# Kernel tuning notes

Hardware: AMD Instinct MI355X
Metric: run time of the kernel (lower is better)

## Reference

```python
import jax, jax.numpy as jnp
import numpy as np

# Forest of complete L-ary trees, BFS level-contiguous node numbering.
B_TREES, ARITY, DEPTH = 8, 4, 8
C, M, NGEN = 8, 100, 4
COUNTS = [B_TREES * ARITY**l for l in range(DEPTH + 1)]
OFFS = np.concatenate([[0], np.cumsum(COUNTS)]).astype(np.int64)
DIM = int(OFFS[-1])  # 699048
# tree id of each node: within-level index // (ARITY**level)
BATCH = np.concatenate([np.arange(COUNTS[l]) // (ARITY**l) for l in range(DEPTH + 1)])


def setup_inputs() -> dict:
    key = jax.random.key(0)
    k1, k2, k3, k4 = jax.random.split(key, 4)
    return {
        "x": jax.random.randint(k1, (DIM,), 0, M, dtype=jnp.int32),
        "A": jax.random.normal(k2, (C, C, ARITY, NGEN), dtype=jnp.float32) * 2.5,
        "B_emit": jax.random.normal(k3, (C, M, NGEN), dtype=jnp.float32) * 2.5,
        "Pi": jax.random.normal(k4, (C, NGEN), dtype=jnp.float32) * 2.5,
    }


def _htmm_loglik(x, A, B_emit, Pi):
    # softmax reparameterization (matches F.softmax axes in torch code)
    smA = jax.nn.softmax(A, axis=0)            # [C,C,L,G], over child state
    smA_t = jnp.transpose(smA, (2, 0, 1, 3))   # [L,C,C,G]
    smB = jax.nn.softmax(B_emit, axis=1)       # [C,M,G]
    smPi = jax.nn.softmax(Pi, axis=0)          # [C,G]

    # preliminary downward: prior state distribution per node, level by level.
    # Children of a parent are contiguous with sibling position j = idx % ARITY.
    prior_lvls = [jnp.broadcast_to(smPi, (COUNTS[0], C, NGEN))]
    for l in range(1, DEPTH + 1):
        n_pa = COUNTS[l - 1]
        # prior_child[c] = sum_d A[c, d, pos_j, g] * prior_pa[d]
        pl = jnp.einsum('jcdg,pdg->pjcg', smA_t, prior_lvls[-1])
        prior_lvls.append(pl.reshape(n_pa * ARITY, C, NGEN))
    prior = jnp.concatenate(prior_lvls, axis=0)  # [DIM,C,G]

    em = jnp.transpose(smB[:, x], (1, 0, 2))     # [DIM,C,G]
    beta0 = prior * em

    ll = jnp.zeros((DIM, NGEN), dtype=beta0.dtype)
    # leaves = deepest level
    beta_lvl = beta0[OFFS[DEPTH]:OFFS[DEPTH + 1]]
    nu = beta_lvl.sum(1)                          # [n_leaves,G]
    beta_lvl = beta_lvl / nu[:, None, :]
    ll = ll.at[OFFS[DEPTH]:OFFS[DEPTH + 1]].set(jnp.log(nu))

    # upward recursion, bottom-up
    for l in range(DEPTH, 0, -1):
        n_pa = COUNTS[l - 1]
        ratio = (beta_lvl / prior[OFFS[l]:OFFS[l + 1]]).reshape(n_pa, ARITY, C, NGEN)
        # beta_uv[d] = sum_c A[c, d, pos_j, g] * beta_ch[c] / prior_ch[c]
        beta_uv = jnp.einsum('jcdg,pjcg->pjdg', smA_t, ratio)  # [n_pa,L,C,G]
        beta_pa = beta0[OFFS[l - 1]:OFFS[l]] * jnp.prod(beta_uv, axis=1)
        nu = beta_pa.sum(1)
        beta_lvl = beta_pa / nu[:, None, :]
        ll = ll.at[OFFS[l - 1]:OFFS[l]].set(jnp.log(nu))

    # scatter per-node log-likelihood contributions into per-tree totals
    return jax.ops.segment_sum(ll, jnp.asarray(BATCH), num_segments=B_TREES)  # [B_TREES,G]


def reference(x, A, B_emit, Pi):
    return _htmm_loglik(x, A, B_emit, Pi)
```

## Files before the change

kernel.cpp:

```cpp
#include <hip/hip_runtime.h>

constexpr int OFFS1 = 8, OFFS2 = 40, OFFS3 = 168, OFFS4 = 680;
constexpr int OFFS5 = 2728, OFFS6 = 10920, OFFS7 = 43688, OFFS8 = 174760;


template <int CTRL>
static __device__ __forceinline__ float dppmov(float v) {
  return __int_as_float(__builtin_amdgcn_update_dpp(0, __float_as_int(v), CTRL, 0xF, 0xF, true));
}

static __device__ __forceinline__ float bfly8(float v) {
  v += dppmov<0xB1>(v);
  v += dppmov<0x4E>(v);
  v += dppmov<0x141>(v);
  return v;
}

static __device__ __forceinline__ void oct8(float v, float pv[8]) {
  float m = dppmov<0x141>(v);
  pv[0] = dppmov<0x00>(v); pv[1] = dppmov<0x55>(v);
  pv[2] = dppmov<0xAA>(v); pv[3] = dppmov<0xFF>(v);
  pv[4] = dppmov<0x00>(m); pv[5] = dppmov<0x55>(m);
  pv[6] = dppmov<0xAA>(m); pv[7] = dppmov<0xFF>(m);
}

static __device__ __forceinline__ float dot8(const float w[8], const float v[8]) {
  return w[0]*v[0] + w[1]*v[1] + w[2]*v[2] + w[3]*v[3] +
         w[4]*v[4] + w[5]*v[5] + w[6]*v[6] + w[7]*v[7];
}

static __device__ __forceinline__ void ld8p(const float* p, float wp[8], int h) {
  const float4* q = (const float4*)p;
  float4 a = q[h], b = q[1 - h];
  wp[0] = a.x; wp[1] = a.y; wp[2] = a.z; wp[3] = a.w;
  wp[4] = b.w; wp[5] = b.z; wp[6] = b.y; wp[7] = b.x;
}

static __device__ __forceinline__ float dot8p(const float wp[8], const float* p, int h) {
  const float4* q = (const float4*)p;
  float4 a = q[h], b = q[1 - h];
  return wp[0]*a.x + wp[1]*a.y + wp[2]*a.z + wp[3]*a.w +
         wp[4]*b.w + wp[5]*b.z + wp[6]*b.y + wp[7]*b.x;
}

static __device__ __forceinline__ float dot8pT(const float wp[8], const float* row, int h) {
  const float2* q = (const float2*)row;
  float2 a = q[2 * h], b = q[2 * h + 1], c = q[3 - 2 * h], d = q[2 - 2 * h];
  return wp[0]*a.x + wp[1]*a.y + wp[2]*b.x + wp[3]*b.y +
         wp[4]*c.y + wp[5]*c.x + wp[6]*d.y + wp[7]*d.x;
}

static __device__ __forceinline__ float rcpf(float x) { return __builtin_amdgcn_rcpf(x); }

static __device__ __forceinline__ float step_downT(const float* wtdT, float v, int j,
                                                   int sg, int h) {
  float pv[8];
  oct8(v, pv);
  return dot8pT(pv, &wtdT[(j * 32 + sg) * 10], h);
}

static __device__ __forceinline__ float step_down(const float* wtd_l, float v, int j,
                                                  int r, int h) {
  const float* wb = &wtd_l[j * 256 + r];
  float w[8];
#pragma unroll
  for (int k = 0; k < 4; k++) {
    w[k]     = wb[(4 * h + k) * 32];
    w[4 + k] = wb[(7 - 4 * h - k) * 32];
  }
  float pv[8];
  oct8(v, pv);
  return dot8(w, pv);
}

static __device__ __forceinline__ float upprod(const float wup_p[4][8], const float rat[4]) {
  float prod = 1.f;
#pragma unroll
  for (int j = 0; j < 4; j++) {
    float pr[8];
    oct8(rat[j], pr);
    prod *= dot8(wup_p[j], pr);
  }
  return prod;
}

static __device__ __forceinline__ float leaf7(float u7, float e0, float e1, float e2,
                                              float e3, float em, float* acc) {
  float n0 = bfly8(u7 * e0), n1 = bfly8(u7 * e1);
  float n2 = bfly8(u7 * e2), n3 = bfly8(u7 * e3);
  float p01 = n0 * n1, p23 = n2 * n3;
  float prod = (e0 * e1 * rcpf(p01)) * (e2 * e3 * rcpf(p23));
  *acc += __logf(p01) + __logf(p23);
  float nu7 = bfly8(u7 * em * prod);
  *acc += __logf(nu7);
  return em * prod * rcpf(nu7);
}

static __device__ __forceinline__ void build_tables(const float* __restrict__ A,
                                                    const float* __restrict__ Bm,
                                                    const float* __restrict__ Pi,
                                                    float* wtd_l, float* emt_l,
                                                    float* pit_l, float* llb, int t) {
  if (t < 128) {
    int d = t >> 4, j = (t >> 2) & 3, gg = t & 3;
    float v[8], sum = 0.f;
#pragma unroll
    for (int ss = 0; ss < 8; ss++) { v[ss] = __expf(A[((ss * 8 + d) * 4 + j) * 4 + gg]); sum += v[ss]; }
    float inv = rcpf(sum);
#pragma unroll
    for (int ss = 0; ss < 8; ss++) wtd_l[(j * 8 + d) * 32 + gg * 8 + ss] = v[ss] * inv;
  }
  if (t < 4) {
    float v[8], sum = 0.f;
#pragma unroll
    for (int c = 0; c < 8; c++) { v[c] = __expf(Pi[c * 4 + t]); sum += v[c]; }
    float inv = rcpf(sum);
#pragma unroll
    for (int c = 0; c < 8; c++) pit_l[t * 8 + c] = v[c] * inv;
    llb[t] = 0.f;
  }
  {
    int row = t >> 3, part = t & 7, c = row >> 2, gg = row & 3;
    int m0 = part < 4 ? part * 13 : 52 + (part - 4) * 12;
    int mn = part < 4 ? 13 : 12;
    float sum = 0.f;
    for (int m = m0; m < m0 + mn; m++) sum += __expf(Bm[(c * 100 + m) * 4 + gg]);
    sum = bfly8(sum);
    float inv = rcpf(sum);
    for (int m = m0; m < m0 + mn; m++)
      emt_l[m * 32 + gg * 8 + c] = __expf(Bm[(c * 100 + m) * 4 + gg]) * inv;
  }
}

__global__ __launch_bounds__(256, 2) void k_phase1(const int* __restrict__ x,
                                                   const float* __restrict__ A,
                                                   const float* __restrict__ Bm,
                                                   const float* __restrict__ Pi,
                                                   float* __restrict__ RAT4,
                                                   float* __restrict__ blocksum) {
  __shared__ __align__(16) float wtd_l[1024];
  __shared__ __align__(16) float wtdT[1280];
  __shared__ __align__(16) float emt_l[3200];
  __shared__ __align__(16) float pit_l[32];
  __shared__ __align__(16) float xb[320];
  __shared__ float llb[4];

  int t = threadIdx.x;
  int r = t & 31, g = r >> 3, s = r & 7, grp = t >> 5;
  int h = s >> 2, gb = g * 8;
  int sg = s * 4 + g;
  int b = blockIdx.x;

  build_tables(A, Bm, Pi, wtd_l, emt_l, pit_l, llb, t);
  __syncthreads();
  if (t < 128) {
    int j = t >> 5, ss = (t >> 2) & 7, gg = t & 3;
#pragma unroll
    for (int d = 0; d < 8; d++) wtdT[t * 10 + d] = wtd_l[(j * 8 + d) * 32 + gg * 8 + ss];
  }
  float wup_p[4][8];
#pragma unroll
  for (int j = 0; j < 4; j++) ld8p(&wtd_l[(j * 8 + s) * 32 + gb], wup_p[j], h);
  __syncthreads();

  float acc = 0.f;
  {
    int n5 = b * 8 + grp;
    const int4* x8v = (const int4*)(x + OFFS8 + n5 * 64);
    const int4* x7p = (const int4*)(x + OFFS7 + n5 * 16);
    int4 x6v = *(const int4*)(x + OFFS6 + n5 * 4);
    int x5s = x[OFFS5 + n5];
    const int* x6a = (const int*)&x6v;

    float v5 = pit_l[r], pri4 = 0.f;
#pragma unroll
    for (int k = 1; k <= 5; k++) {
      v5 = step_downT(wtdT, v5, (n5 >> (2 * (5 - k))) & 3, sg, h);
      if (k == 4) pri4 = v5;
    }
    float pv5[8];
    oct8(v5, pv5);

    float rat6[4];
#pragma unroll
    for (int q6 = 0; q6 < 4; q6++) {
      float u6 = dot8pT(pv5, &wtdT[(q6 * 32 + sg) * 10], h);
      float pv6[8];
      oct8(u6, pv6);
      int4 x7q = x7p[q6];
      const int* x7a = (const int*)&x7q;

      float rat7[4];
#pragma unroll
      for (int q7 = 0; q7 < 4; q7++) {
        int4 xl = x8v[q6 * 4 + q7];
        const int* xa = (const int*)&xl;
        float E[4];
#pragma unroll
        for (int j = 0; j < 4; j++) E[j] = dot8p(wup_p[j], &emt_l[xa[j] * 32 + gb], h);
        float u7 = dot8pT(pv6, &wtdT[(q7 * 32 + sg) * 10], h);
        rat7[q7] = leaf7(u7, E[0], E[1], E[2], E[3], emt_l[x7a[q7] * 32 + r], &acc);
      }
      float prod6 = upprod(wup_p, rat7);
      float em6 = emt_l[x6a[q6] * 32 + r];
      float nu6 = bfly8(u6 * em6 * prod6);
      acc += __logf(nu6);
      rat6[q6] = em6 * prod6 * rcpf(nu6);
    }
    float prod5 = upprod(wup_p, rat6);
    float em5 = emt_l[x5s * 32 + r];
    float nu5 = bfly8(v5 * em5 * prod5);
    acc += __logf(nu5);
    xb[grp * 32 + r] = em5 * prod5 * rcpf(nu5);
    if ((grp & 3) == 0) xb[256 + (grp >> 2) * 32 + r] = pri4;
  }
  __syncthreads();

  if (grp < 2) {
    int n4 = b * 2 + grp;
    float prod = 1.f;
#pragma unroll
    for (int j = 0; j < 4; j++) prod *= dot8p(wup_p[j], &xb[(grp * 4 + j) * 32 + gb], h);
    float em = emt_l[x[OFFS4 + n4] * 32 + r];
    float pr4 = xb[256 + grp * 32 + r];
    float nu = bfly8(pr4 * em * prod);
    acc += __logf(nu);
    RAT4[n4 * 32 + r] = em * prod * rcpf(nu);
  }

  if (s == 0) atomicAdd(&llb[g], acc);
  __syncthreads();
  if (t < 4) blocksum[b * 4 + t] = llb[t];
}

__global__ __launch_bounds__(256) void k_phase2(const int* __restrict__ x,
                                                const float* __restrict__ A,
                                                const float* __restrict__ Bm,
                                                const float* __restrict__ Pi,
                                                const float* __restrict__ RAT4,
                                                const float* __restrict__ blocksum,
                                                float* __restrict__ out) {
  __shared__ __align__(16) float wtd_l[1024];
  __shared__ __align__(16) float emt_l[3200];
  __shared__ __align__(16) float pit_l[32];
  __shared__ __align__(16) float stg[8192];
  __shared__ __align__(16) float xb[640];
  __shared__ float llb[4];

  int t = threadIdx.x;
  int r = t & 31, g = r >> 3, s = r & 7, grp = t >> 5;
  int h = s >> 2, gb = g * 8;
  int tree = blockIdx.x;

  build_tables(A, Bm, Pi, wtd_l, emt_l, pit_l, llb, t);
  {
    const float4* src = (const float4*)(RAT4 + tree * 8192);
    float4* dst = (float4*)stg;
#pragma unroll
    for (int i = 0; i < 8; i++) dst[i * 256 + t] = src[i * 256 + t];
  }
  __syncthreads();

  float wtd_p[4][8], wup_p[4][8];
#pragma unroll
  for (int j = 0; j < 4; j++) {
    const float* wb = &wtd_l[j * 256 + r];
#pragma unroll
    for (int k = 0; k < 4; k++) {
      wtd_p[j][k]     = wb[(4 * h + k) * 32];
      wtd_p[j][4 + k] = wb[(7 - 4 * h - k) * 32];
    }
    ld8p(&wtd_l[(j * 8 + s) * 32 + gb], wup_p[j], h);
  }

  float acc2 = 0.f;
  {
    int n2A = tree * 16 + grp, n2B = n2A + 8;
    int4 x3A = *(const int4*)(x + OFFS3 + n2A * 4);
    int4 x3B = *(const int4*)(x + OFFS3 + n2B * 4);
    int x2A = x[OFFS2 + n2A], x2B = x[OFFS2 + n2B];
    const int* xa = (const int*)&x3A;
    const int* xbv = (const int*)&x3B;
    float v2A = pit_l[r], v2B = v2A;
    v2A = step_down(wtd_l, v2A, (n2A >> 2) & 3, r, h);
    v2B = step_down(wtd_l, v2B, (n2B >> 2) & 3, r, h);
    v2A = step_down(wtd_l, v2A, n2A & 3, r, h);
    v2B = step_down(wtd_l, v2B, n2B & 3, r, h);
    float pv2A[8], pv2B[8];
    oct8(v2A, pv2A); oct8(v2B, pv2B);
    float rat3A[4], rat3B[4];
#pragma unroll
    for (int j3 = 0; j3 < 4; j3++) {
      int i3A = grp * 4 + j3, i3B = (8 + grp) * 4 + j3;
      float p3A = dot8(wtd_p[j3], pv2A);
      float p3B = dot8(wtd_p[j3], pv2B);
      float prodA = 1.f, prodB = 1.f;
#pragma unroll
      for (int j = 0; j < 4; j++) {
        prodA *= dot8p(wup_p[j], &stg[(i3A * 4 + j) * 32 + gb], h);
        prodB *= dot8p(wup_p[j], &stg[(i3B * 4 + j) * 32 + gb], h);
      }
      float emA = emt_l[xa[j3] * 32 + r], emB = emt_l[xbv[j3] * 32 + r];
      float nuA = bfly8(p3A * emA * prodA), nuB = bfly8(p3B * emB * prodB);
      acc2 += __logf(nuA) + __logf(nuB);
      rat3A[j3] = emA * prodA * rcpf(nuA);
      rat3B[j3] = emB * prodB * rcpf(nuB);
    }
    float prodA = upprod(wup_p, rat3A);
    float prodB = upprod(wup_p, rat3B);
    float emA = emt_l[x2A * 32 + r], emB = emt_l[x2B * 32 + r];
    float nuA = bfly8(v2A * emA * prodA), nuB = bfly8(v2B * emB * prodB);
    acc2 += __logf(nuA) + __logf(nuB);
    xb[grp * 32 + r] = emA * prodA * rcpf(nuA);
    xb[(8 + grp) * 32 + r] = emB * prodB * rcpf(nuB);
  }
  __syncthreads();
  if (grp < 4) {
    int n1g = tree * 4 + grp;
    float v1 = step_down(wtd_l, pit_l[r], grp, r, h);
    float prod = 1.f;
#pragma unroll
    for (int j = 0; j < 4; j++) prod *= dot8p(wup_p[j], &xb[(grp * 4 + j) * 32 + gb], h);
    float em = emt_l[x[OFFS1 + n1g] * 32 + r];
    float nu = bfly8(v1 * em * prod);
    acc2 += __logf(nu);
    xb[512 + grp * 32 + r] = em * prod * rcpf(nu);
  }
  __syncthreads();
  if (grp == 0) {
    float pr = pit_l[r];
    float prod = 1.f;
#pragma unroll
    for (int j = 0; j < 4; j++) prod *= dot8p(wup_p[j], &xb[512 + j * 32 + gb], h);
    float em = emt_l[x[tree] * 32 + r];
    float nu = bfly8(pr * em * prod);
    acc2 += __logf(nu);
  }
  __syncthreads();
  if (s == 0) atomicAdd(&llb[g], acc2);
  float v = blocksum[tree * 512 + t] + blocksum[tree * 512 + 256 + t];
  __syncthreads();
  stg[t] = v;
  __syncthreads();
#pragma unroll
  for (int off = 128; off >= 4; off >>= 1) {
    if (t < off) stg[t] += stg[t + off];
    __syncthreads();
  }
  if (t < 4) out[tree * 4 + t] = stg[t] + llb[t];
}

extern "C" void kernel_launch(void* const* d_in, const int* in_sizes, int n_in,
                              void* d_out, int out_size, void* d_ws, size_t ws_size,
                              hipStream_t stream) {
  const int* x = (const int*)d_in[0];
  const float* A = (const float*)d_in[1];
  const float* Bm = (const float*)d_in[2];
  const float* Pi = (const float*)d_in[3];
  float* ws = (float*)d_ws;
  float* blocksum = ws + 256;
  float* RAT4 = ws + 256 + 4096;
  float* out = (float*)d_out;

  k_phase1<<<1024, 256, 0, stream>>>(x, A, Bm, Pi, RAT4, blocksum);
  k_phase2<<<8, 256, 0, stream>>>(x, A, Bm, Pi, RAT4, blocksum, out);
}
```

Measured before the change: 100.1 us.

## Stage x indices in LDS, stream upward products, and stop unrolling phase1 loops

Phase1 now loads the block's x indices for levels 5-8 into shared memory with coalesced loads at the start, instead of issuing per-wave int4 global loads inside the loop. The upward product is accumulated on the fly with a new transposed wupT table and DPP broadcasts, so the rat7/rat6 arrays are no longer kept, and the nested loops are marked unroll 1. The aim is lower register pressure and fewer scattered global loads, at the cost of more LDS use, more LDS reads, and loop overhead.

```diff
diff --git a/kernel.cpp b/kernel.cpp
--- a/kernel.cpp
+++ b/kernel.cpp
@@ -140,8 +140,10 @@
                                                    float* __restrict__ blocksum) {
   __shared__ __align__(16) float wtd_l[1024];
   __shared__ __align__(16) float wtdT[1280];
+  __shared__ __align__(16) float wupT[1280];
   __shared__ __align__(16) float emt_l[3200];
   __shared__ __align__(16) float pit_l[32];
+  __shared__ __align__(16) int   xle[680];
   __shared__ __align__(16) float xb[320];
   __shared__ float llb[4];
 
@@ -152,11 +154,19 @@
   int b = blockIdx.x;
 
   build_tables(A, Bm, Pi, wtd_l, emt_l, pit_l, llb, t);
+  xle[t] = x[OFFS8 + b * 512 + t];
+  xle[256 + t] = x[OFFS8 + b * 512 + 256 + t];
+  if (t < 128) xle[512 + t] = x[OFFS7 + b * 128 + t];
+  if (t < 32) xle[640 + t] = x[OFFS6 + b * 32 + t];
+  if (t < 8) xle[672 + t] = x[OFFS5 + b * 8 + t];
   __syncthreads();
   if (t < 128) {
     int j = t >> 5, ss = (t >> 2) & 7, gg = t & 3;
 #pragma unroll
-    for (int d = 0; d < 8; d++) wtdT[t * 10 + d] = wtd_l[(j * 8 + d) * 32 + gg * 8 + ss];
+    for (int d = 0; d < 8; d++) {
+      wtdT[t * 10 + d] = wtd_l[(j * 8 + d) * 32 + gg * 8 + ss];
+      wupT[t * 10 + d] = wtd_l[(j * 8 + ss) * 32 + gg * 8 + d];
+    }
   }
   float wup_p[4][8];
 #pragma unroll
@@ -164,56 +174,51 @@
   __syncthreads();
 
   float acc = 0.f;
-  {
-    int n5 = b * 8 + grp;
-    const int4* x8v = (const int4*)(x + OFFS8 + n5 * 64);
-    const int4* x7p = (const int4*)(x + OFFS7 + n5 * 16);
-    int4 x6v = *(const int4*)(x + OFFS6 + n5 * 4);
-    int x5s = x[OFFS5 + n5];
-    const int* x6a = (const int*)&x6v;
-
-    float v5 = pit_l[r], pri4 = 0.f;
-#pragma unroll
-    for (int k = 1; k <= 5; k++) {
-      v5 = step_downT(wtdT, v5, (n5 >> (2 * (5 - k))) & 3, sg, h);
-      if (k == 4) pri4 = v5;
+  int n5 = b * 8 + grp;
+
+  float v5 = pit_l[r], pri4 = 0.f;
+#pragma unroll 1
+  for (int k = 1; k <= 5; k++) {
+    v5 = step_downT(wtdT, v5, (n5 >> (2 * (5 - k))) & 3, sg, h);
+    if (k == 4) pri4 = v5;
+  }
+  float pv5[8];
+  oct8(v5, pv5);
+
+  float prod5 = 1.f;
+#pragma unroll 1
+  for (int q6 = 0; q6 < 4; q6++) {
+    float u6 = dot8pT(pv5, &wtdT[(q6 * 32 + sg) * 10], h);
+    float pv6[8];
+    oct8(u6, pv6);
+    float prod6 = 1.f;
+#pragma unroll 1
+    for (int q7 = 0; q7 < 4; q7++) {
+      int4 xl = ((const int4*)xle)[grp * 16 + q6 * 4 + q7];
+      const int* xa = (const int*)&xl;
+      float E[4];
+#pragma unroll
+      for (int j = 0; j < 4; j++) E[j] = dot8p(wup_p[j], &emt_l[xa[j] * 32 + gb], h);
+      float u7 = dot8pT(pv6, &wtdT[(q7 * 32 + sg) * 10], h);
+      float em7 = emt_l[xle[512 + grp * 16 + q6 * 4 + q7] * 32 + r];
+      float rat7 = leaf7(u7, E[0], E[1], E[2], E[3], em7, &acc);
+      float pr[8];
+      oct8(rat7, pr);
+      prod6 *= dot8pT(pr, &wupT[(q7 * 32 + sg) * 10], h);
     }
-    float pv5[8];
-    oct8(v5, pv5);
-
-    float rat6[4];
-#pragma unroll
-    for (int q6 = 0; q6 < 4; q6++) {
-      float u6 = dot8pT(pv5, &wtdT[(q6 * 32 + sg) * 10], h);
-      float pv6[8];
-      oct8(u6, pv6);
-      int4 x7q = x7p[q6];
-      const int* x7a = (const int*)&x7q;
-
-      float rat7[4];
-#pragma unroll
-      for (int q7 = 0; q7 < 4; q7++) {
-        int4 xl = x8v[q6 * 4 + q7];
-        const int* xa = (const int*)&xl;
-        float E[4];
-#pragma unroll
-        for (int j = 0; j < 4; j++) E[j] = dot8p(wup_p[j], &emt_l[xa[j] * 32 + gb], h);
-        float u7 = dot8pT(pv6, &wtdT[(q7 * 32 + sg) * 10], h);
-        rat7[q7] = leaf7(u7, E[0], E[1], E[2], E[3], emt_l[x7a[q7] * 32 + r], &acc);
-      }
-      float prod6 = upprod(wup_p, rat7);
-      float em6 = emt_l[x6a[q6] * 32 + r];
-      float nu6 = bfly8(u6 * em6 * prod6);
-      acc += __logf(nu6);
-      rat6[q6] = em6 * prod6 * rcpf(nu6);
-    }
-    float prod5 = upprod(wup_p, rat6);
-    float em5 = emt_l[x5s * 32 + r];
-    float nu5 = bfly8(v5 * em5 * prod5);
-    acc += __logf(nu5);
-    xb[grp * 32 + r] = em5 * prod5 * rcpf(nu5);
-    if ((grp & 3) == 0) xb[256 + (grp >> 2) * 32 + r] = pri4;
-  }
+    float em6 = emt_l[xle[640 + grp * 4 + q6] * 32 + r];
+    float nu6 = bfly8(u6 * em6 * prod6);
+    acc += __logf(nu6);
+    float rat6 = em6 * prod6 * rcpf(nu6);
+    float pr6[8];
+    oct8(rat6, pr6);
+    prod5 *= dot8pT(pr6, &wupT[(q6 * 32 + sg) * 10], h);
+  }
+  float em5 = emt_l[xle[672 + grp] * 32 + r];
+  float nu5 = bfly8(v5 * em5 * prod5);
+  acc += __logf(nu5);
+  xb[grp * 32 + r] = em5 * prod5 * rcpf(nu5);
+  if ((grp & 3) == 0) xb[256 + (grp >> 2) * 32 + r] = pri4;
   __syncthreads();
 
   if (grp < 2) {
```

Result: no change. 101.3 us (+1.2%).

## Precompute leaf emission-transition table in LDS and halve phase1 grid

Applied to the files above, without the earlier changes.

Builds a per-block shared table of transition-weighted leaf emissions (symbol × sibling position), so each leaf's E term becomes a single LDS lookup instead of an 8-wide dot product. Down-step weights are now kept in registers, replacing the transposed wtdT table. Each block processes two rounds of level-5 subtrees, with the grid halved to 512, which amortises the table build over more work. The cost is a larger LDS footprint (about 50KB more) that may reduce occupancy below two blocks per CU, extra per-block table construction, and more register pressure from the wtd_p array.

```diff
diff --git a/kernel.cpp b/kernel.cpp
--- a/kernel.cpp
+++ b/kernel.cpp
@@ -29,6 +29,13 @@
          w[4]*v[4] + w[5]*v[5] + w[6]*v[6] + w[7]*v[7];
 }
 
+static __device__ __forceinline__ void ld8(const float* p, float pv[8]) {
+  const float4* q = (const float4*)p;
+  float4 a = q[0], b = q[1];
+  pv[0] = a.x; pv[1] = a.y; pv[2] = a.z; pv[3] = a.w;
+  pv[4] = b.x; pv[5] = b.y; pv[6] = b.z; pv[7] = b.w;
+}
+
 static __device__ __forceinline__ void ld8p(const float* p, float wp[8], int h) {
   const float4* q = (const float4*)p;
   float4 a = q[h], b = q[1 - h];
@@ -43,21 +50,14 @@
          wp[4]*b.w + wp[5]*b.z + wp[6]*b.y + wp[7]*b.x;
 }
 
-static __device__ __forceinline__ float dot8pT(const float wp[8], const float* row, int h) {
-  const float2* q = (const float2*)row;
-  float2 a = q[2 * h], b = q[2 * h + 1], c = q[3 - 2 * h], d = q[2 - 2 * h];
-  return wp[0]*a.x + wp[1]*a.y + wp[2]*b.x + wp[3]*b.y +
-         wp[4]*c.y + wp[5]*c.x + wp[6]*d.y + wp[7]*d.x;
+static __device__ __forceinline__ float dot8r(const float w[8], const float* p) {
+  const float4* q = (const float4*)p;
+  float4 a = q[0], b = q[1];
+  return w[0]*a.x + w[1]*a.y + w[2]*a.z + w[3]*a.w +
+         w[4]*b.x + w[5]*b.y + w[6]*b.z + w[7]*b.w;
 }
 
 static __device__ __forceinline__ float rcpf(float x) { return __builtin_amdgcn_rcpf(x); }
-
-static __device__ __forceinline__ float step_downT(const float* wtdT, float v, int j,
-                                                   int sg, int h) {
-  float pv[8];
-  oct8(v, pv);
-  return dot8pT(pv, &wtdT[(j * 32 + sg) * 10], h);
-}
 
 static __device__ __forceinline__ float step_down(const float* wtd_l, float v, int j,
                                                   int r, int h) {
@@ -139,33 +139,45 @@
                                                    float* __restrict__ RAT4,
                                                    float* __restrict__ blocksum) {
   __shared__ __align__(16) float wtd_l[1024];
-  __shared__ __align__(16) float wtdT[1280];
   __shared__ __align__(16) float emt_l[3200];
+  __shared__ __align__(16) float etab_l[12800];
   __shared__ __align__(16) float pit_l[32];
-  __shared__ __align__(16) float xb[320];
+  __shared__ __align__(16) float rat5buf[16][32];
+  __shared__ __align__(16) float pri4buf[4][32];
   __shared__ float llb[4];
 
   int t = threadIdx.x;
   int r = t & 31, g = r >> 3, s = r & 7, grp = t >> 5;
   int h = s >> 2, gb = g * 8;
-  int sg = s * 4 + g;
   int b = blockIdx.x;
 
   build_tables(A, Bm, Pi, wtd_l, emt_l, pit_l, llb, t);
   __syncthreads();
-  if (t < 128) {
-    int j = t >> 5, ss = (t >> 2) & 7, gg = t & 3;
-#pragma unroll
-    for (int d = 0; d < 8; d++) wtdT[t * 10 + d] = wtd_l[(j * 8 + d) * 32 + gg * 8 + ss];
-  }
-  float wup_p[4][8];
-#pragma unroll
-  for (int j = 0; j < 4; j++) ld8p(&wtd_l[(j * 8 + s) * 32 + gb], wup_p[j], h);
+  {
+    int c7 = t & 127, half = t >> 7;
+    int j = c7 >> 5, d = (c7 >> 2) & 7, gg = c7 & 3;
+    float w[8];
+    ld8(&wtd_l[(j * 8 + d) * 32 + gg * 8], w);
+    for (int m = half * 50; m < half * 50 + 50; m++)
+      etab_l[(m * 4 + j) * 32 + gg * 8 + d] = dot8r(w, &emt_l[m * 32 + gg * 8]);
+  }
+  float wtd_p[4][8], wup_p[4][8];
+#pragma unroll
+  for (int j = 0; j < 4; j++) {
+    const float* wb = &wtd_l[j * 256 + r];
+#pragma unroll
+    for (int k = 0; k < 4; k++) {
+      wtd_p[j][k]     = wb[(4 * h + k) * 32];
+      wtd_p[j][4 + k] = wb[(7 - 4 * h - k) * 32];
+    }
+    ld8p(&wtd_l[(j * 8 + s) * 32 + gb], wup_p[j], h);
+  }
   __syncthreads();
 
   float acc = 0.f;
-  {
-    int n5 = b * 8 + grp;
+#pragma unroll 1
+  for (int round = 0; round < 2; round++) {
+    int n5 = b * 16 + round * 8 + grp;
     const int4* x8v = (const int4*)(x + OFFS8 + n5 * 64);
     const int4* x7p = (const int4*)(x + OFFS7 + n5 * 16);
     int4 x6v = *(const int4*)(x + OFFS6 + n5 * 4);
@@ -175,7 +187,7 @@
     float v5 = pit_l[r], pri4 = 0.f;
 #pragma unroll
     for (int k = 1; k <= 5; k++) {
-      v5 = step_downT(wtdT, v5, (n5 >> (2 * (5 - k))) & 3, sg, h);
+      v5 = step_down(wtd_l, v5, (n5 >> (2 * (5 - k))) & 3, r, h);
       if (k == 4) pri4 = v5;
     }
     float pv5[8];
@@ -184,7 +196,7 @@
     float rat6[4];
 #pragma unroll
     for (int q6 = 0; q6 < 4; q6++) {
-      float u6 = dot8pT(pv5, &wtdT[(q6 * 32 + sg) * 10], h);
+      float u6 = dot8(wtd_p[q6], pv5);
       float pv6[8];
       oct8(u6, pv6);
       int4 x7q = x7p[q6];
@@ -197,8 +209,8 @@
         const int* xa = (const int*)&xl;
         float E[4];
 #pragma unroll
-        for (int j = 0; j < 4; j++) E[j] = dot8p(wup_p[j], &emt_l[xa[j] * 32 + gb], h);
-        float u7 = dot8pT(pv6, &wtdT[(q7 * 32 + sg) * 10], h);
+        for (int j = 0; j < 4; j++) E[j] = etab_l[(xa[j] * 4 + j) * 32 + r];
+        float u7 = dot8(wtd_p[q7], pv6);
         rat7[q7] = leaf7(u7, E[0], E[1], E[2], E[3], emt_l[x7a[q7] * 32 + r], &acc);
       }
       float prod6 = upprod(wup_p, rat7);
@@ -211,18 +223,18 @@
     float em5 = emt_l[x5s * 32 + r];
     float nu5 = bfly8(v5 * em5 * prod5);
     acc += __logf(nu5);
-    xb[grp * 32 + r] = em5 * prod5 * rcpf(nu5);
-    if ((grp & 3) == 0) xb[256 + (grp >> 2) * 32 + r] = pri4;
-  }
-  __syncthreads();
-
-  if (grp < 2) {
-    int n4 = b * 2 + grp;
+    rat5buf[round * 8 + grp][r] = em5 * prod5 * rcpf(nu5);
+    if ((grp & 3) == 0) pri4buf[round * 2 + (grp >> 2)][r] = pri4;
+  }
+  __syncthreads();
+
+  if (grp < 4) {
+    int n4 = b * 4 + grp;
     float prod = 1.f;
 #pragma unroll
-    for (int j = 0; j < 4; j++) prod *= dot8p(wup_p[j], &xb[(grp * 4 + j) * 32 + gb], h);
+    for (int j = 0; j < 4; j++) prod *= dot8p(wup_p[j], &rat5buf[grp * 4 + j][gb], h);
     float em = emt_l[x[OFFS4 + n4] * 32 + r];
-    float pr4 = xb[256 + grp * 32 + r];
+    float pr4 = pri4buf[grp][r];
     float nu = bfly8(pr4 * em * prod);
     acc += __logf(nu);
     RAT4[n4 * 32 + r] = em * prod * rcpf(nu);
@@ -338,7 +350,7 @@
   }
   __syncthreads();
   if (s == 0) atomicAdd(&llb[g], acc2);
-  float v = blocksum[tree * 512 + t] + blocksum[tree * 512 + 256 + t];
+  float v = blocksum[tree * 256 + t];
   __syncthreads();
   stg[t] = v;
   __syncthreads();
@@ -359,9 +371,9 @@
   const float* Pi = (const float*)d_in[3];
   float* ws = (float*)d_ws;
   float* blocksum = ws + 256;
-  float* RAT4 = ws + 256 + 4096;
+  float* RAT4 = ws + 256 + 2048;
   float* out = (float*)d_out;
 
-  k_phase1<<<1024, 256, 0, stream>>>(x, A, Bm, Pi, RAT4, blocksum);
+  k_phase1<<<512, 256, 0, stream>>>(x, A, Bm, Pi, RAT4, blocksum);
   k_phase2<<<8, 256, 0, stream>>>(x, A, Bm, Pi, RAT4, blocksum, out);
 }
```

Result: faster. 94.52 us (-5.6%).
